# Kernel tuning notes

Hardware: AMD Instinct MI355X
Metric: run time of the kernel (lower is better)

## Reference

```python
import math
import jax, jax.numpy as jnp
import numpy as np

EMBED_DIM = 768
NUM_HEADS = 12
HEAD_DIM = EMBED_DIM // NUM_HEADS


def setup_inputs() -> dict:
    key = jax.random.key(0)
    ks = jax.random.split(key, 9)
    R, C, B, E = 128, 512, 1, EMBED_DIM
    x = jax.random.normal(ks[0], (R, C, B, E), dtype=jnp.float32)
    s = 0.02
    # weights stored so that projection is x @ W + b (i.e. torch Linear weight transposed)
    Wq = jax.random.normal(ks[1], (E, E), dtype=jnp.float32) * s
    Wk = jax.random.normal(ks[2], (E, E), dtype=jnp.float32) * s
    Wv = jax.random.normal(ks[3], (E, E), dtype=jnp.float32) * s
    Wo = jax.random.normal(ks[4], (E, E), dtype=jnp.float32) * s
    bq = jnp.zeros((E,), jnp.float32)
    bk = jnp.zeros((E,), jnp.float32)
    bv = jnp.zeros((E,), jnp.float32)
    bo = jnp.zeros((E,), jnp.float32)
    return {"x": x, "Wq": Wq, "bq": bq, "Wk": Wk, "bk": bk,
            "Wv": Wv, "bv": bv, "Wo": Wo, "bo": bo}


def reference(x, Wq, bq, Wk, bk, Wv, bv, Wo, bo):
    R, C, B, E = x.shape
    H, D = NUM_HEADS, HEAD_DIM
    # scaling = head_dim^-0.5 / sqrt(num_rows)  (align_scaling)
    scaling = (D ** -0.5) / math.sqrt(R)
    q = (x @ Wq + bq).reshape(R, C, B, H, D) * scaling
    k = (x @ Wk + bk).reshape(R, C, B, H, D)
    v = (x @ Wv + bv).reshape(R, C, B, H, D)
    # sum attention logits over rows r -> shared [h, n, i, j] attention map
    attn_weights = jnp.einsum('rinhd,rjnhd->hnij', q, k)
    attn_probs = jax.nn.softmax(attn_weights, axis=-1)
    context = jnp.einsum('hnij,rjnhd->rinhd', attn_probs, v)
    context = context.reshape(R, C, B, E)
    output = context @ Wo + bo
    return output, attn_probs
```

## Files before the change

kernel.cpp:

```cpp
#include <hip/hip_runtime.h>
#include <math.h>

#define RDIM 128
#define CDIM 512
#define EDIM 768
#define HDIM 12
#define DDIM 64
#define MDIM (RDIM*CDIM)
#define OUT_ELEMS ((size_t)MDIM*EDIM)
#define HSTRIDE ((size_t)CDIM*RDIM*DDIM)
#define WELEMS (EDIM*EDIM)

typedef unsigned short ushort_t;
typedef __attribute__((ext_vector_type(8))) short bf16x8;
typedef __attribute__((ext_vector_type(8))) unsigned short u16x8;
typedef __attribute__((ext_vector_type(4))) float f32x4;

__device__ __forceinline__ ushort_t f2bf(float f) {
    unsigned u = __float_as_uint(f);
    unsigned r = u + 0x7fffu + ((u >> 16) & 1u);
    return (ushort_t)(r >> 16);
}

__device__ __forceinline__ void gload16(const void* g, void* l) {
    __builtin_amdgcn_global_load_lds(
        (const __attribute__((address_space(1))) unsigned int*)g,
        (__attribute__((address_space(3))) unsigned int*)l, 16, 0, 0);
}

__global__ __launch_bounds__(256)
void cast_x(const float* __restrict__ x, ushort_t* __restrict__ xb) {
    size_t i = ((size_t)blockIdx.x * 256 + threadIdx.x) * 8;
    float4 a = *(const float4*)&x[i];
    float4 b = *(const float4*)&x[i + 4];
    u16x8 o;
    o[0]=f2bf(a.x); o[1]=f2bf(a.y); o[2]=f2bf(a.z); o[3]=f2bf(a.w);
    o[4]=f2bf(b.x); o[5]=f2bf(b.y); o[6]=f2bf(b.z); o[7]=f2bf(b.w);
    *(u16x8*)&xb[i] = o;
}

__global__ __launch_bounds__(256)
void transpose_cast_w(const float* __restrict__ W, ushort_t* __restrict__ Wt) {
    __shared__ ushort_t t[64][66];
    const int k0 = blockIdx.x * 64, n0 = blockIdx.y * 64;
    const int tx = threadIdx.x & 15, ty = threadIdx.x >> 4;
    #pragma unroll
    for (int rep = 0; rep < 4; ++rep) {
        int k = ty + rep * 16;
        float4 v = *(const float4*)&W[(size_t)(k0 + k) * EDIM + n0 + tx*4];
        t[k][tx*4+0] = f2bf(v.x); t[k][tx*4+1] = f2bf(v.y);
        t[k][tx*4+2] = f2bf(v.z); t[k][tx*4+3] = f2bf(v.w);
    }
    __syncthreads();
    #pragma unroll
    for (int rep = 0; rep < 4; ++rep) {
        int n = ty + rep * 16;
        ushort4 o = { t[tx*4+0][n], t[tx*4+1][n], t[tx*4+2][n], t[tx*4+3][n] };
        *(ushort4*)&Wt[(size_t)(n0 + n) * EDIM + k0 + tx*4] = o;
    }
}

__global__ __launch_bounds__(256)
void concat_bias(const float* __restrict__ bq, const float* __restrict__ bk,
                 const float* __restrict__ bv, float* __restrict__ bqkv) {
    int i = blockIdx.x * 256 + threadIdx.x;
    if (i < 768)        bqkv[i] = bq[i];
    else if (i < 1536)  bqkv[i] = bk[i - 768];
    else if (i < 2304)  bqkv[i] = bv[i - 1536];
}

#define SBAR do { __builtin_amdgcn_sched_barrier(0); \
                  __builtin_amdgcn_s_barrier(); \
                  __builtin_amdgcn_sched_barrier(0); } while(0)
#define LGKM0 do { asm volatile("s_waitcnt lgkmcnt(0)" ::: "memory"); \
                   __builtin_amdgcn_sched_barrier(0); } while(0)
#define VMCNT(n_) asm volatile("s_waitcnt vmcnt(" #n_ ")" ::: "memory")

template<int M, int N, int K, int LDK, int MODE, int NWG>
__global__ __launch_bounds__(512, 2)
void gemm8(const ushort_t* __restrict__ A, const ushort_t* __restrict__ B,
           const float* __restrict__ bias, float scale,
           float* __restrict__ outF, ushort_t* __restrict__ outB,
           size_t sAh, size_t sBh) {
    __shared__ __align__(16) char smem[131072];
    constexpr int NT = K / 64;

    const int tid = threadIdx.x;
    const int lane = tid & 63, wid = tid >> 6;
    const int wr = wid >> 2, wc = wid & 3;
    const int fr = lane & 15, fs = lane >> 4;
    const int sw = (fr & 7) << 3;

    const int bid = blockIdx.x;
    const int w = (bid & 7) * (NWG / 8) + (bid >> 3);
    int bm, bn, h = 0, ksub = 0, plane = 0, ntile = 0;
    if (MODE == 4)      { ntile = w % 9; bm = (w / 9) * 256; bn = ntile * 256; }
    else if (MODE == 2) { plane = w >> 2; h = plane >> 2; ksub = plane & 3;
                          bm = ((w >> 1) & 1) * 256; bn = (w & 1) * 256; }
    else if (MODE == 3) { h = w >> 6; bm = ((w >> 5) & 1) * 256; bn = (w & 31) * 256; }
    else                { bm = (w / 3) * 256; bn = (w % 3) * 256; }

    const ushort_t* Ab = A + (MODE == 2 || MODE == 3 ? (size_t)h * sAh : 0)
                       + (MODE == 2 ? (size_t)ksub * 2048 : 0) + (size_t)bm * LDK;
    const ushort_t* Bb = B + (MODE == 2 || MODE == 3 ? (size_t)h * sBh : 0)
                       + (MODE == 2 ? (size_t)ksub * 2048 : 0) + (size_t)bn * LDK;

    const int r0 = tid >> 3, s0 = tid & 7;
    const size_t gO0 = (size_t)r0 * LDK + ((s0 ^ (r0 & 7)) * 8);
    const size_t gO1 = gO0 + (size_t)64 * LDK;
    const int l0 = tid * 16, l1 = tid * 16 + 8192;

#define STAGE_A(t_, h_) do { \
    char* d_ = smem + ((((t_) & 1) * 2 + (h_)) * 16384); \
    const ushort_t* s_ = Ab + (size_t)((h_) * 128) * LDK + (t_) * 64; \
    gload16(s_ + gO0, d_ + l0); gload16(s_ + gO1, d_ + l1); } while(0)
#define STAGE_B(t_, h_) do { \
    char* d_ = smem + 65536 + ((((t_) & 1) * 2 + (h_)) * 16384); \
    const ushort_t* s_ = Bb + (size_t)((h_) * 128) * LDK + (t_) * 64; \
    gload16(s_ + gO0, d_ + l0); gload16(s_ + gO1, d_ + l1); } while(0)

    f32x4 acc[8][4];
    #pragma unroll
    for (int i = 0; i < 8; ++i)
        #pragma unroll
        for (int j = 0; j < 4; ++j) acc[i][j] = (f32x4){0.f, 0.f, 0.f, 0.f};
    bf16x8 a_[4][2], bb_[4][2];

#define DSA(t_, mq_) do { \
    const ushort_t* As_ = (const ushort_t*)(smem + ((((t_) & 1) * 2 + wr) * 16384)); \
    _Pragma("unroll") for (int f = 0; f < 4; ++f) \
      _Pragma("unroll") for (int kk = 0; kk < 2; ++kk) \
        a_[f][kk] = *(const bf16x8*)&As_[((mq_) * 64 + f * 16 + fr) * 64 \
                                          + ((kk * 32 + fs * 8) ^ sw)]; } while(0)

#define DSB(t_) do { \
    const ushort_t* Bs_ = (const ushort_t*)(smem + 65536 + ((((t_) & 1) * 2 + (wc >> 1)) * 16384)); \
    _Pragma("unroll") for (int nf = 0; nf < 4; ++nf) \
      _Pragma("unroll") for (int kk = 0; kk < 2; ++kk) \
        bb_[nf][kk] = *(const bf16x8*)&Bs_[((wc & 1) * 64 + nf * 16 + fr) * 64 \
                                            + ((kk * 32 + fs * 8) ^ sw)]; } while(0)

#define MFMA8(mq_, nq_) do { \
    __builtin_amdgcn_s_setprio(1); \
    _Pragma("unroll") for (int f = 0; f < 4; ++f) \
      _Pragma("unroll") for (int nf2 = 0; nf2 < 2; ++nf2) \
        _Pragma("unroll") for (int kk = 0; kk < 2; ++kk) \
          acc[(mq_) * 4 + f][(nq_) * 2 + nf2] = __builtin_amdgcn_mfma_f32_16x16x32_bf16( \
              a_[f][kk], bb_[(nq_) * 2 + nf2][kk], acc[(mq_) * 4 + f][(nq_) * 2 + nf2], 0, 0, 0); \
    __builtin_amdgcn_s_setprio(0); } while(0)

    STAGE_B(0, 0); __builtin_amdgcn_sched_barrier(0);
    STAGE_B(0, 1); __builtin_amdgcn_sched_barrier(0);
    STAGE_A(0, 0); __builtin_amdgcn_sched_barrier(0);
    STAGE_A(0, 1); __builtin_amdgcn_sched_barrier(0);
    STAGE_B(1, 0); __builtin_amdgcn_sched_barrier(0);
    STAGE_B(1, 1); __builtin_amdgcn_sched_barrier(0);
    STAGE_A(1, 0); __builtin_amdgcn_sched_barrier(0);
    STAGE_A(1, 1); __builtin_amdgcn_sched_barrier(0);
    VMCNT(8);
    SBAR;

    for (int t = 0; t < NT - 2; ++t) {
        DSA(t, 0); DSB(t);
        LGKM0; MFMA8(0, 0); SBAR;
        STAGE_B(t + 2, 0);
        MFMA8(0, 1); SBAR;
        DSA(t, 1);
        STAGE_B(t + 2, 1);
        LGKM0; MFMA8(1, 0); SBAR;
        STAGE_A(t + 2, 0); STAGE_A(t + 2, 1);
        MFMA8(1, 1);
        VMCNT(8);
        SBAR;
    }

    #pragma unroll
    for (int tt = 0; tt < 2; ++tt) {
        const int t = NT - 2 + tt;
        if (tt == 1) { VMCNT(0); SBAR; }
        DSA(t, 0); DSB(t);
        LGKM0; MFMA8(0, 0); SBAR;
        MFMA8(0, 1); SBAR;
        DSA(t, 1);
        LGKM0; MFMA8(1, 0); SBAR;
        MFMA8(1, 1); SBAR;
    }

    if (MODE == 4) {
        const int which = ntile / 3;
        const int hcb = (ntile % 3) * 256;
        if (which < 2) {
            ushort_t* dst = outB + (size_t)which * OUT_ELEMS;
            const float sc = (which == 0) ? scale : 1.f;
            #pragma unroll
            for (int mf = 0; mf < 8; ++mf) {
                #pragma unroll
                for (int nf = 0; nf < 4; ++nf) {
                    const int hcol = hcb + wc*64 + nf*16 + fr;
                    const float bv = bias[which*768 + hcol];
                    const int hh = hcol >> 6, d = hcol & 63;
                    #pragma unroll
                    for (int j = 0; j < 4; ++j) {
                        const int m = bm + wr*128 + mf*16 + fs*4 + j;
                        float v = (acc[mf][nf][j] + bv) * sc;
                        size_t addr = (size_t)hh * HSTRIDE
                                    + (size_t)(m & 511) * 8192 + (m >> 9) * 64 + d;
                        dst[addr] = f2bf(v);
                    }
                }
            }
        } else {
            ushort_t* Ts = (ushort_t*)smem;
            ushort_t* dst = outB + 2 * OUT_ELEMS;
            const int rblk = bm >> 9, jb = bm & 511;
            __syncthreads();
            #pragma unroll
            for (int q = 0; q < 2; ++q) {
                if ((wc >> 1) == q) {
                    #pragma unroll
                    for (int mf = 0; mf < 8; ++mf) {
                        #pragma unroll
                        for (int nf = 0; nf < 4; ++nf) {
                            const int nl = wc*64 + nf*16 + fr;
                            const float bv = bias[1536 + hcb + nl];
                            #pragma unroll
                            for (int j = 0; j < 4; ++j)
                                Ts[(nl & 127)*264 + wr*128 + mf*16 + fs*4 + j] =
                                    f2bf(acc[mf][nf][j] + bv);
                        }
                    }
                }
                __syncthreads();
                #pragma unroll
                for (int it = 0; it < 8; ++it) {
                    const int idx = it * 512 + tid;
                    const int row = idx >> 5, c8 = (idx & 31) * 8;
                    const int nl = q*128 + row;
                    const int hh = (hcb + nl) >> 6, d = nl & 63;
                    uint4 wv;
                    wv.x = *(const uint*)&Ts[row*264 + c8];
                    wv.y = *(const uint*)&Ts[row*264 + c8 + 2];
                    wv.z = *(const uint*)&Ts[row*264 + c8 + 4];
                    wv.w = *(const uint*)&Ts[row*264 + c8 + 6];
                    size_t addr = (size_t)hh * HSTRIDE
                                + (size_t)(rblk*64 + d) * CDIM + jb + c8;
                    *(uint4*)&dst[addr] = wv;
                }
                __syncthreads();
            }
        }
        return;
    }

    #pragma unroll
    for (int mf = 0; mf < 8; ++mf) {
        #pragma unroll
        for (int nf = 0; nf < 4; ++nf) {
            const int n = bn + wc*64 + nf*16 + fr;
            float bv = (MODE == 1) ? bias[n] : 0.f;
            #pragma unroll
            for (int j = 0; j < 4; ++j) {
                const int m = bm + wr*128 + mf*16 + fs*4 + j;
                float v = acc[mf][nf][j];
                if (MODE == 1) {
                    outF[(size_t)m * N + n] = v + bv;
                } else if (MODE == 2) {
                    outF[(size_t)plane * (CDIM*CDIM) + (size_t)m * CDIM + n] = v;
                } else {
                    size_t addr = ((size_t)(n >> 6) * CDIM + m) * EDIM
                                + h * DDIM + (n & 63);
                    outB[addr] = f2bf(v);
                }
            }
        }
    }
}

__global__ __launch_bounds__(256)
void softmax_reduce(const float* __restrict__ part, float* __restrict__ attn,
                    ushort_t* __restrict__ Pb) {
    const int row = blockIdx.x;
    const int h = row >> 9, c = row & 511;
    const int tid = threadIdx.x;
    const int lane = tid & 63, wid = tid >> 6;
    __shared__ float red[8];

    float v0 = 0.f, v1 = 0.f;
    #pragma unroll
    for (int s = 0; s < 4; ++s) {
        const float* p = part + ((size_t)(h*4 + s) * (CDIM*CDIM)) + (size_t)c * CDIM;
        v0 += p[tid];
        v1 += p[tid + 256];
    }
    float m = fmaxf(v0, v1);
    #pragma unroll
    for (int off = 32; off > 0; off >>= 1) m = fmaxf(m, __shfl_down(m, off));
    if (lane == 0) red[wid] = m;
    __syncthreads();
    if (tid == 0) red[4] = fmaxf(fmaxf(red[0], red[1]), fmaxf(red[2], red[3]));
    __syncthreads();
    const float M = red[4];

    float e0 = expf(v0 - M), e1 = expf(v1 - M);
    float s = e0 + e1;
    #pragma unroll
    for (int off = 32; off > 0; off >>= 1) s += __shfl_down(s, off);
    __syncthreads();
    if (lane == 0) red[wid] = s;
    __syncthreads();
    if (tid == 0) red[5] = red[0] + red[1] + red[2] + red[3];
    __syncthreads();
    const float inv = 1.f / red[5];
    float o0 = e0 * inv, o1 = e1 * inv;
    float* pout = attn + (size_t)row * CDIM;
    ushort_t* pb = Pb + (size_t)row * CDIM;
    pout[tid] = o0;        pout[tid + 256] = o1;
    pb[tid]   = f2bf(o0);  pb[tid + 256]   = f2bf(o1);
}

extern "C" void kernel_launch(void* const* d_in, const int* in_sizes, int n_in,
                              void* d_out, int out_size, void* d_ws, size_t ws_size,
                              hipStream_t stream) {
    const float* x  = (const float*)d_in[0];
    const float* Wq = (const float*)d_in[1];
    const float* bq = (const float*)d_in[2];
    const float* Wk = (const float*)d_in[3];
    const float* bk = (const float*)d_in[4];
    const float* Wv = (const float*)d_in[5];
    const float* bv = (const float*)d_in[6];
    const float* Wo = (const float*)d_in[7];
    const float* bo = (const float*)d_in[8];

    float* out   = (float*)d_out;
    float* attnp = out + OUT_ELEMS;

    ushort_t* ws   = (ushort_t*)d_ws;
    ushort_t* xb   = ws;
    ushort_t* Wqkv = xb + OUT_ELEMS;
    ushort_t* Wto  = Wqkv + 3*WELEMS;
    float*    bqkv = (float*)(Wto + WELEMS);
    ushort_t* Qp   = Wto + WELEMS + 4608;
    ushort_t* Kp   = Qp + OUT_ELEMS;
    ushort_t* Vt   = Kp + OUT_ELEMS;
    ushort_t* Pb   = Vt + OUT_ELEMS;
    float*    part = (float*)(Pb + (size_t)HDIM*CDIM*CDIM);
    ushort_t* ctxb = xb;

    const float scaling = 0.011048543456039806f;

    cast_x<<<MDIM*EDIM/(256*8), 256, 0, stream>>>(x, xb);
    dim3 wt(EDIM/64, EDIM/64);
    transpose_cast_w<<<wt, 256, 0, stream>>>(Wq, Wqkv);
    transpose_cast_w<<<wt, 256, 0, stream>>>(Wk, Wqkv + WELEMS);
    transpose_cast_w<<<wt, 256, 0, stream>>>(Wv, Wqkv + 2*WELEMS);
    transpose_cast_w<<<wt, 256, 0, stream>>>(Wo, Wto);
    concat_bias<<<9, 256, 0, stream>>>(bq, bk, bv, bqkv);

    gemm8<MDIM, 2304, EDIM, EDIM, 4, 2304><<<2304, 512, 0, stream>>>(
        xb, Wqkv, bqkv, scaling, nullptr, Qp, 0, 0);

    gemm8<CDIM, CDIM, 2048, 8192, 2, 192><<<192, 512, 0, stream>>>(
        Qp, Kp, nullptr, 1.f, part, nullptr, HSTRIDE, HSTRIDE);

    softmax_reduce<<<HDIM*CDIM, 256, 0, stream>>>(part, attnp, Pb);

    gemm8<CDIM, 8192, CDIM, CDIM, 3, 768><<<768, 512, 0, stream>>>(
        Pb, Vt, nullptr, 1.f, nullptr, ctxb, (size_t)CDIM*CDIM, HSTRIDE);

    gemm8<MDIM, EDIM, EDIM, EDIM, 1, 768><<<768, 512, 0, stream>>>(
        ctxb, Wto, bo, 1.f, out, nullptr, 0, 0);
}
```

Measured before the change: 587.8 us.

## Double split-K for QK logits GEMM and restructure B-fragment LDS loads

The QK-logits GEMM now splits its K reduction into 8 partial slices instead of 4, launching 384 workgroups instead of 192 so more compute units stay busy. The softmax reduction sums 8 partials to match, and the partials buffer now reuses the x-cast workspace. The GEMM main loop splits its B-fragment LDS reads into two halves issued just before their MFMAs and drops the explicit lgkmcnt waits, relying on compiler-inserted waits to overlap LDS reads with compute. The finer split adds partial-sum traffic in the softmax pass, and aliasing the partials with xb assumes xb is dead by then.

After: 581.8 us. Within noise of the previous version (-1.0%).

```diff
diff --git a/kernel.cpp b/kernel.cpp
--- a/kernel.cpp
+++ b/kernel.cpp
@@ -72,8 +72,7 @@
 #define SBAR do { __builtin_amdgcn_sched_barrier(0); \
                   __builtin_amdgcn_s_barrier(); \
                   __builtin_amdgcn_sched_barrier(0); } while(0)
-#define LGKM0 do { asm volatile("s_waitcnt lgkmcnt(0)" ::: "memory"); \
-                   __builtin_amdgcn_sched_barrier(0); } while(0)
+#define SCHED0 __builtin_amdgcn_sched_barrier(0)
 #define VMCNT(n_) asm volatile("s_waitcnt vmcnt(" #n_ ")" ::: "memory")
 
 template<int M, int N, int K, int LDK, int MODE, int NWG>
@@ -95,15 +94,15 @@
     const int w = (bid & 7) * (NWG / 8) + (bid >> 3);
     int bm, bn, h = 0, ksub = 0, plane = 0, ntile = 0;
     if (MODE == 4)      { ntile = w % 9; bm = (w / 9) * 256; bn = ntile * 256; }
-    else if (MODE == 2) { plane = w >> 2; h = plane >> 2; ksub = plane & 3;
+    else if (MODE == 2) { plane = w >> 2; h = plane >> 3; ksub = plane & 7;
                           bm = ((w >> 1) & 1) * 256; bn = (w & 1) * 256; }
     else if (MODE == 3) { h = w >> 6; bm = ((w >> 5) & 1) * 256; bn = (w & 31) * 256; }
     else                { bm = (w / 3) * 256; bn = (w % 3) * 256; }
 
     const ushort_t* Ab = A + (MODE == 2 || MODE == 3 ? (size_t)h * sAh : 0)
-                       + (MODE == 2 ? (size_t)ksub * 2048 : 0) + (size_t)bm * LDK;
+                       + (MODE == 2 ? (size_t)ksub * K : 0) + (size_t)bm * LDK;
     const ushort_t* Bb = B + (MODE == 2 || MODE == 3 ? (size_t)h * sBh : 0)
-                       + (MODE == 2 ? (size_t)ksub * 2048 : 0) + (size_t)bn * LDK;
+                       + (MODE == 2 ? (size_t)ksub * K : 0) + (size_t)bn * LDK;
 
     const int r0 = tid >> 3, s0 = tid & 7;
     const size_t gO0 = (size_t)r0 * LDK + ((s0 ^ (r0 & 7)) * 8);
@@ -124,7 +123,7 @@
     for (int i = 0; i < 8; ++i)
         #pragma unroll
         for (int j = 0; j < 4; ++j) acc[i][j] = (f32x4){0.f, 0.f, 0.f, 0.f};
-    bf16x8 a_[4][2], bb_[4][2];
+    bf16x8 a_[4][2], bb0_[2][2], bb1_[2][2];
 
 #define DSA(t_, mq_) do { \
     const ushort_t* As_ = (const ushort_t*)(smem + ((((t_) & 1) * 2 + wr) * 16384)); \
@@ -133,57 +132,63 @@
         a_[f][kk] = *(const bf16x8*)&As_[((mq_) * 64 + f * 16 + fr) * 64 \
                                           + ((kk * 32 + fs * 8) ^ sw)]; } while(0)
 
-#define DSB(t_) do { \
+#define DSB(t_, nq_, B_) do { \
     const ushort_t* Bs_ = (const ushort_t*)(smem + 65536 + ((((t_) & 1) * 2 + (wc >> 1)) * 16384)); \
-    _Pragma("unroll") for (int nf = 0; nf < 4; ++nf) \
+    _Pragma("unroll") for (int nf = 0; nf < 2; ++nf) \
       _Pragma("unroll") for (int kk = 0; kk < 2; ++kk) \
-        bb_[nf][kk] = *(const bf16x8*)&Bs_[((wc & 1) * 64 + nf * 16 + fr) * 64 \
-                                            + ((kk * 32 + fs * 8) ^ sw)]; } while(0)
-
-#define MFMA8(mq_, nq_) do { \
+        B_[nf][kk] = *(const bf16x8*)&Bs_[((wc & 1) * 64 + (nq_) * 32 + nf * 16 + fr) * 64 \
+                                           + ((kk * 32 + fs * 8) ^ sw)]; } while(0)
+
+#define MFMA8(mq_, nq_, B_) do { \
     __builtin_amdgcn_s_setprio(1); \
     _Pragma("unroll") for (int f = 0; f < 4; ++f) \
       _Pragma("unroll") for (int nf2 = 0; nf2 < 2; ++nf2) \
         _Pragma("unroll") for (int kk = 0; kk < 2; ++kk) \
           acc[(mq_) * 4 + f][(nq_) * 2 + nf2] = __builtin_amdgcn_mfma_f32_16x16x32_bf16( \
-              a_[f][kk], bb_[(nq_) * 2 + nf2][kk], acc[(mq_) * 4 + f][(nq_) * 2 + nf2], 0, 0, 0); \
+              a_[f][kk], B_[nf2][kk], acc[(mq_) * 4 + f][(nq_) * 2 + nf2], 0, 0, 0); \
     __builtin_amdgcn_s_setprio(0); } while(0)
 
-    STAGE_B(0, 0); __builtin_amdgcn_sched_barrier(0);
-    STAGE_B(0, 1); __builtin_amdgcn_sched_barrier(0);
-    STAGE_A(0, 0); __builtin_amdgcn_sched_barrier(0);
-    STAGE_A(0, 1); __builtin_amdgcn_sched_barrier(0);
-    STAGE_B(1, 0); __builtin_amdgcn_sched_barrier(0);
-    STAGE_B(1, 1); __builtin_amdgcn_sched_barrier(0);
-    STAGE_A(1, 0); __builtin_amdgcn_sched_barrier(0);
-    STAGE_A(1, 1); __builtin_amdgcn_sched_barrier(0);
+    STAGE_B(0, 0); SCHED0;
+    STAGE_B(0, 1); SCHED0;
+    STAGE_A(0, 0); SCHED0;
+    STAGE_A(0, 1); SCHED0;
+    STAGE_B(1, 0); SCHED0;
+    STAGE_B(1, 1); SCHED0;
+    STAGE_A(1, 0); SCHED0;
+    STAGE_A(1, 1); SCHED0;
     VMCNT(8);
     SBAR;
 
     for (int t = 0; t < NT - 2; ++t) {
-        DSA(t, 0); DSB(t);
-        LGKM0; MFMA8(0, 0); SBAR;
-        STAGE_B(t + 2, 0);
-        MFMA8(0, 1); SBAR;
+        DSA(t, 0); DSB(t, 0, bb0_);
+        MFMA8(0, 0, bb0_);
+        SBAR;
+        DSB(t, 1, bb1_);
+        MFMA8(0, 1, bb1_);
+        SBAR;
         DSA(t, 1);
-        STAGE_B(t + 2, 1);
-        LGKM0; MFMA8(1, 0); SBAR;
+        STAGE_B(t + 2, 0); STAGE_B(t + 2, 1);
+        MFMA8(1, 0, bb0_);
+        SBAR;
         STAGE_A(t + 2, 0); STAGE_A(t + 2, 1);
-        MFMA8(1, 1);
+        MFMA8(1, 1, bb1_);
         VMCNT(8);
         SBAR;
     }
 
-    #pragma unroll
-    for (int tt = 0; tt < 2; ++tt) {
-        const int t = NT - 2 + tt;
-        if (tt == 1) { VMCNT(0); SBAR; }
-        DSA(t, 0); DSB(t);
-        LGKM0; MFMA8(0, 0); SBAR;
-        MFMA8(0, 1); SBAR;
-        DSA(t, 1);
-        LGKM0; MFMA8(1, 0); SBAR;
-        MFMA8(1, 1); SBAR;
+    {
+        const int t = NT - 2;
+        DSA(t, 0); DSB(t, 0, bb0_); MFMA8(0, 0, bb0_); SBAR;
+        DSB(t, 1, bb1_);            MFMA8(0, 1, bb1_); SBAR;
+        DSA(t, 1);                  MFMA8(1, 0, bb0_); SBAR;
+        MFMA8(1, 1, bb1_);
+        VMCNT(0);
+        SBAR;
+        const int u = NT - 1;
+        DSA(u, 0); DSB(u, 0, bb0_); MFMA8(0, 0, bb0_); SBAR;
+        DSB(u, 1, bb1_);            MFMA8(0, 1, bb1_); SBAR;
+        DSA(u, 1);                  MFMA8(1, 0, bb0_); SBAR;
+        MFMA8(1, 1, bb1_);
     }
 
     if (MODE == 4) {
@@ -287,8 +292,8 @@
 
     float v0 = 0.f, v1 = 0.f;
     #pragma unroll
-    for (int s = 0; s < 4; ++s) {
-        const float* p = part + ((size_t)(h*4 + s) * (CDIM*CDIM)) + (size_t)c * CDIM;
+    for (int s = 0; s < 8; ++s) {
+        const float* p = part + ((size_t)(h*8 + s) * (CDIM*CDIM)) + (size_t)c * CDIM;
         v0 += p[tid];
         v1 += p[tid + 256];
     }
@@ -343,7 +348,7 @@
     ushort_t* Kp   = Qp + OUT_ELEMS;
     ushort_t* Vt   = Kp + OUT_ELEMS;
     ushort_t* Pb   = Vt + OUT_ELEMS;
-    float*    part = (float*)(Pb + (size_t)HDIM*CDIM*CDIM);
+    float*    part = (float*)xb;
     ushort_t* ctxb = xb;
 
     const float scaling = 0.011048543456039806f;
@@ -359,7 +364,7 @@
     gemm8<MDIM, 2304, EDIM, EDIM, 4, 2304><<<2304, 512, 0, stream>>>(
         xb, Wqkv, bqkv, scaling, nullptr, Qp, 0, 0);
 
-    gemm8<CDIM, CDIM, 2048, 8192, 2, 192><<<192, 512, 0, stream>>>(
+    gemm8<CDIM, CDIM, 1024, 8192, 2, 384><<<384, 512, 0, stream>>>(
         Qp, Kp, nullptr, 1.f, part, nullptr, HSTRIDE, HSTRIDE);
 
     softmax_reduce<<<HDIM*CDIM, 256, 0, stream>>>(part, attnp, Pb);
```
